# Kernel tuning notes

Measured on AMD Instinct MI355X. Metric: run time of the kernel, lower is better.

## Reference

```python
import jax, jax.numpy as jnp
import numpy as np

B, H, W = 64, 512, 512
T = 100           # num_thresholds
R = 8             # defect regions per image (max label id)
BLOCK = 128       # defect regions are 128x128 blocks on a 4x4 grid
SAT = 1.0         # saturation_threshold (relative)


def setup_inputs() -> dict:
    key = jax.random.key(0)
    k1, _ = jax.random.split(key)
    preds = jax.random.uniform(k1, (B, H, W), dtype=jnp.float32)
    thresholds = jnp.linspace(0.0, 1.0, T).astype(jnp.float32)
    # Build a labeled GT mask: R disjoint 128x128 block regions per image,
    # labels 1..R (0 = background). This plays the role of measure.label(target).
    rng = np.random.default_rng(0)
    labels = np.zeros((B, H, W), dtype=np.int32)
    gb = H // BLOCK           # 4 blocks per side -> 16 candidate blocks
    nblocks = gb * gb
    for b in range(B):
        chosen = rng.permutation(nblocks)[:R]
        for rid, blk in enumerate(chosen, start=1):
            r, c = divmod(int(blk), gb)
            labels[b, r * BLOCK:(r + 1) * BLOCK, c * BLOCK:(c + 1) * BLOCK] = rid
    return {"preds": preds, "thresholds": thresholds, "labels": jnp.asarray(labels)}


def reference(preds, thresholds, labels):
    # preds: (B,H,W) float32 in [0,1); thresholds: (T,) sorted; labels: (B,H,W) int32, 0=bg.
    Bn, Hn, Wn = preds.shape
    Tn = thresholds.shape[0]
    flat_s = preds.reshape(-1)
    flat_l = labels.reshape(-1)
    # bucket[p] = number of thresholds <= score[p]; pixel passes thr[t] iff bucket > t.
    bucket = jnp.searchsorted(thresholds, flat_s, side='right')  # int in [0, T]
    # ---- background FP / TN per threshold (exact counts via histogram) ----
    bg = (flat_l == 0).astype(jnp.int32)
    bg_hist = jax.ops.segment_sum(bg, bucket, num_segments=Tn + 1)  # (T+1,)
    bg_total = bg_hist.sum()
    fp = (bg_total - jnp.cumsum(bg_hist)[:Tn]).astype(jnp.float32)  # fp[t] = #bg with score>=thr[t]
    tn = bg_total.astype(jnp.float32) - fp
    # ---- per-region TP per threshold (segmented histogram) ----
    bidx = jnp.repeat(jnp.arange(Bn), Hn * Wn)
    seg = bidx * R + (flat_l - 1)              # region id in [0, B*R)
    comb = seg * (Tn + 1) + bucket
    NSEG = Bn * R * (Tn + 1)
    comb = jnp.where(flat_l > 0, comb, NSEG)   # dump bg pixels in overflow slot
    hist = jax.ops.segment_sum(jnp.ones_like(bucket, dtype=jnp.int32), comb,
                               num_segments=NSEG + 1)[:NSEG].reshape(Bn, R, Tn + 1)
    area = hist.sum(-1)                                       # (B,R) defect areas
    tp = (area[..., None] - jnp.cumsum(hist, -1)[..., :Tn]).astype(jnp.float32)  # (B,R,T)
    sat = jnp.maximum(area.astype(jnp.float32) * SAT, 1.0)    # relative saturation
    valid = (area > 0).astype(jnp.float32)                    # guard empty regions
    spro = jnp.minimum(tp / sat[..., None], 1.0) * valid[..., None]
    spro_sum = spro.sum((0, 1))                               # (T,)
    n_def = jnp.maximum(valid.sum(), 1.0)
    mean_spro = spro_sum / n_def
    # ---- AUC over FPR (max_fpr = 1.0) ----
    denom = fp + tn
    fpr = jnp.where(denom > 0, fp / jnp.maximum(denom, 1.0), 0.0)
    order = jnp.argsort(fpr)
    x = fpr[order]
    y = mean_spro[order]
    auc = jnp.sum((x[1:] - x[:-1]) * (y[1:] + y[:-1]) * 0.5)  # trapezoid rule
    return auc
```

## Files before the change

### kernel.cpp

```cpp
#include <hip/hip_runtime.h>

#define B_N 64
#define H_N 512
#define W_N 512
#define T_N 100
#define TB  101
#define R_N 8
#define NLAB 9
#define BLOCKS_PER_IMG 16
#define PIX_PER_IMG (H_N * W_N)
#define PIX_PER_BLOCK (PIX_PER_IMG / BLOCKS_PER_IMG)

__global__ __launch_bounds__(256) void hist_kernel(
    const float* __restrict__ preds, const int* __restrict__ labels,
    const float* __restrict__ thr,
    int* __restrict__ region_hist,
    int* __restrict__ bg_hist)
{
    __shared__ float s_thr[T_N];
    __shared__ int whist[4][NLAB * TB];

    const int tid  = threadIdx.x;
    const int wave = tid >> 6;

    for (int i = tid; i < 4 * NLAB * TB; i += 256) ((int*)whist)[i] = 0;
    if (tid < T_N) s_thr[tid] = thr[tid];
    __syncthreads();

    const int img   = blockIdx.x / BLOCKS_PER_IMG;
    const int chunk = blockIdx.x % BLOCKS_PER_IMG;
    const long base = (long)img * PIX_PER_IMG + (long)chunk * PIX_PER_BLOCK;
    const float4* p4 = (const float4*)(preds + base);
    const int4*   l4 = (const int4*)(labels + base);
    int* __restrict__ myh = whist[wave];

    const int iters = PIX_PER_BLOCK / (256 * 4);
    for (int it = 0; it < iters; ++it) {
        float4 pv = p4[it * 256 + tid];
        int4   lv = l4[it * 256 + tid];
        float ps[4] = {pv.x, pv.y, pv.z, pv.w};
        int   ls[4] = {lv.x, lv.y, lv.z, lv.w};
#pragma unroll
        for (int j = 0; j < 4; ++j) {
            float s = ps[j];
            int k = (int)(s * (float)(T_N - 1)) + 1;
            k = max(0, min(T_N, k));
            while (k < T_N && s_thr[k] <= s) ++k;
            while (k > 0 && s_thr[k - 1] > s) --k;
            atomicAdd(&myh[ls[j] * TB + k], 1);
        }
    }
    __syncthreads();

    for (int i = tid; i < NLAB * TB; i += 256) {
        int v = whist[0][i] + whist[1][i] + whist[2][i] + whist[3][i];
        if (v) {
            int lab = i / TB;
            int t   = i - lab * TB;
            if (lab == 0)
                atomicAdd(&bg_hist[img * TB + t], v);
            else
                atomicAdd(&region_hist[(img * R_N + (lab - 1)) * TB + t], v);
        }
    }
}

__global__ __launch_bounds__(128) void region_kernel(
    const int* __restrict__ region_hist,
    float* __restrict__ spro_sum,
    int* __restrict__ n_def)
{
    __shared__ float spro_sh[R_N][T_N];
    __shared__ int validc[R_N];
    const int img = blockIdx.x;
    const int tid = threadIdx.x;

    if (tid < R_N) {
        const int* h = &region_hist[(img * R_N + tid) * TB];
        int area = 0;
        for (int t = 0; t < TB; ++t) area += h[t];
        float sat   = fmaxf((float)area, 1.0f);
        float valid = (area > 0) ? 1.0f : 0.0f;
        int csum = 0;
        for (int t = 0; t < T_N; ++t) {
            csum += h[t];
            float tp = (float)(area - csum);
            spro_sh[tid][t] = fminf(tp / sat, 1.0f) * valid;
        }
        validc[tid] = (area > 0) ? 1 : 0;
    }
    __syncthreads();

    if (tid < T_N) {
        float s = 0.0f;
        for (int r = 0; r < R_N; ++r) s += spro_sh[r][tid];
        atomicAdd(&spro_sum[tid], s);
    }
    if (tid == 0) {
        int v = 0;
        for (int r = 0; r < R_N; ++r) v += validc[r];
        atomicAdd(n_def, v);
    }
}

__global__ __launch_bounds__(128) void final_kernel(
    const int* __restrict__ bg_hist,
    const float* __restrict__ spro_sum,
    const int* __restrict__ n_def,
    float* __restrict__ out)
{
    __shared__ int    bgh[TB];
    __shared__ float  fpr_sh[T_N];
    __shared__ float  ms_sh[T_N];
    __shared__ int    order[T_N];
    __shared__ double contrib[T_N];
    const int tid = threadIdx.x;

    if (tid < TB) {
        int s = 0;
        for (int b = 0; b < B_N; ++b) s += bg_hist[b * TB + tid];
        bgh[tid] = s;
    }
    __syncthreads();

    if (tid < T_N) {
        int fp_i = 0;
        for (int k = tid + 1; k < TB; ++k) fp_i += bgh[k];
        int tot = fp_i;
        for (int k = 0; k <= tid; ++k) tot += bgh[k];
        float bgt = (float)tot;
        float fp  = (float)fp_i;
        fpr_sh[tid] = (bgt > 0.0f) ? fp / fmaxf(bgt, 1.0f) : 0.0f;
        float nd = fmaxf((float)(*n_def), 1.0f);
        ms_sh[tid] = spro_sum[tid] / nd;
    }
    __syncthreads();

    if (tid < T_N) {
        float v = fpr_sh[tid];
        int r = 0;
        for (int j = 0; j < T_N; ++j) {
            float u = fpr_sh[j];
            r += (u < v) | ((u == v) & (j < tid));
        }
        order[r] = tid;
    }
    __syncthreads();

    if (tid < T_N - 1) {
        int o0 = order[tid], o1 = order[tid + 1];
        double x0 = fpr_sh[o0], x1 = fpr_sh[o1];
        double y0 = ms_sh[o0],  y1 = ms_sh[o1];
        contrib[tid] = (x1 - x0) * (y0 + y1) * 0.5;
    } else if (tid < T_N) {
        contrib[tid] = 0.0;
    }
    __syncthreads();

    if (tid == 0) {
        double s = 0.0;
        for (int i = 0; i < T_N - 1; ++i) s += contrib[i];
        out[0] = (float)s;
    }
}

extern "C" void kernel_launch(void* const* d_in, const int* in_sizes, int n_in,
                              void* d_out, int out_size, void* d_ws, size_t ws_size,
                              hipStream_t stream) {
    const float* preds  = (const float*)d_in[0];
    const float* thr    = (const float*)d_in[1];
    const int*   labels = (const int*)d_in[2];
    float* out = (float*)d_out;

    int*   region_hist = (int*)d_ws;
    int*   bg_hist     = region_hist + B_N * R_N * TB;
    float* spro_sum    = (float*)(bg_hist + B_N * TB);
    int*   n_def       = (int*)(spro_sum + T_N);

    size_t zbytes = sizeof(int) * (size_t)(B_N * R_N * TB + B_N * TB)
                  + sizeof(float) * T_N + sizeof(int);
    hipMemsetAsync(d_ws, 0, zbytes, stream);

    hist_kernel<<<B_N * BLOCKS_PER_IMG, 256, 0, stream>>>(preds, labels, thr,
                                                          region_hist, bg_hist);
    region_kernel<<<B_N, 128, 0, stream>>>(region_hist, spro_sum, n_def);
    final_kernel<<<1, 128, 0, stream>>>(bg_hist, spro_sum, n_def, out);
}
```

Baseline: 167.1 us.

## Use LUT bucket lookup, prefetch loads, more chunks, fuse tail kernels

The threshold search now goes through a 256-cell shared-memory table that gives the bucket with one comparison, falling back to a linear scan only near cell edges. The main loop double-buffers its global loads and splits each image into 32 chunks instead of 16, with a launch-bounds occupancy hint. The region and final kernels merge into one single-block tail kernel that reduces across waves with shuffles, removing a launch and the global atomics. The tail now runs on only one block, so its serial work may be slower.

```diff
diff --git a/kernel.cpp b/kernel.cpp
--- a/kernel.cpp
+++ b/kernel.cpp
@@ -7,48 +7,85 @@
 #define TB  101
 #define R_N 8
 #define NLAB 9
-#define BLOCKS_PER_IMG 16
+#define CHUNKS 32
 #define PIX_PER_IMG (H_N * W_N)
-#define PIX_PER_BLOCK (PIX_PER_IMG / BLOCKS_PER_IMG)
-
-__global__ __launch_bounds__(256) void hist_kernel(
+#define CPIX (PIX_PER_IMG / CHUNKS)
+#define NCELL 256
+
+struct LutE { float tlo, thrb, thi; int klo; };
+
+__global__ __launch_bounds__(256, 8) void hist_kernel(
     const float* __restrict__ preds, const int* __restrict__ labels,
     const float* __restrict__ thr,
     int* __restrict__ region_hist,
     int* __restrict__ bg_hist)
 {
     __shared__ float s_thr[T_N];
+    __shared__ __align__(16) LutE lut[NCELL];
     __shared__ int whist[4][NLAB * TB];
 
     const int tid  = threadIdx.x;
     const int wave = tid >> 6;
 
+    if (tid < T_N) s_thr[tid] = thr[tid];
     for (int i = tid; i < 4 * NLAB * TB; i += 256) ((int*)whist)[i] = 0;
-    if (tid < T_N) s_thr[tid] = thr[tid];
-    __syncthreads();
-
-    const int img   = blockIdx.x / BLOCKS_PER_IMG;
-    const int chunk = blockIdx.x % BLOCKS_PER_IMG;
-    const long base = (long)img * PIX_PER_IMG + (long)chunk * PIX_PER_BLOCK;
+    __syncthreads();
+
+    if (tid < NCELL) {
+        float lo = (float)tid * (1.0f / (float)NCELL);
+        int a = 0, b = T_N;
+        while (a < b) { int m = (a + b) >> 1; if (s_thr[m] <= lo) a = m + 1; else b = m; }
+        LutE e;
+        e.tlo  = (a > 0)       ? s_thr[a - 1] : -2.0f;
+        e.thrb = (a < T_N)     ? s_thr[a]     :  2.0f;
+        e.thi  = (a + 1 < T_N) ? s_thr[a + 1] :  2.0f;
+        e.klo  = a;
+        lut[tid] = e;
+    }
+    __syncthreads();
+
+    const int img   = blockIdx.x >> 5;
+    const int chunk = blockIdx.x & (CHUNKS - 1);
+    const long base = (long)img * PIX_PER_IMG + (long)chunk * CPIX;
     const float4* p4 = (const float4*)(preds + base);
     const int4*   l4 = (const int4*)(labels + base);
     int* __restrict__ myh = whist[wave];
 
-    const int iters = PIX_PER_BLOCK / (256 * 4);
-    for (int it = 0; it < iters; ++it) {
-        float4 pv = p4[it * 256 + tid];
-        int4   lv = l4[it * 256 + tid];
+    auto PROC = [&](float4 pv, int4 lv) {
         float ps[4] = {pv.x, pv.y, pv.z, pv.w};
         int   ls[4] = {lv.x, lv.y, lv.z, lv.w};
 #pragma unroll
         for (int j = 0; j < 4; ++j) {
             float s = ps[j];
-            int k = (int)(s * (float)(T_N - 1)) + 1;
-            k = max(0, min(T_N, k));
-            while (k < T_N && s_thr[k] <= s) ++k;
-            while (k > 0 && s_thr[k - 1] > s) --k;
+            int c = (int)(s * (float)NCELL);
+            c = max(0, min(NCELL - 1, c));
+            LutE e = lut[c];
+            bool ge = (s >= e.thrb);
+            int k = e.klo + (ge ? 1 : 0);
+            float lowv  = ge ? e.thrb : e.tlo;
+            float highv = ge ? e.thi  : e.thrb;
+            if (__builtin_expect(!(lowv <= s && s < highv), 0)) {
+                k = max(0, min(T_N, k));
+                while (k < T_N && s_thr[k] <= s) ++k;
+                while (k > 0 && s_thr[k - 1] > s) --k;
+            }
             atomicAdd(&myh[ls[j] * TB + k], 1);
         }
+    };
+
+    float4 pA0 = p4[0 * 256 + tid], pA1 = p4[1 * 256 + tid];
+    int4   lA0 = l4[0 * 256 + tid], lA1 = l4[1 * 256 + tid];
+#pragma unroll
+    for (int g = 0; g < 4; ++g) {
+        float4 pB0, pB1; int4 lB0, lB1;
+        if (g < 3) {
+            const int i0 = (g + 1) * 2;
+            pB0 = p4[(i0    ) * 256 + tid]; pB1 = p4[(i0 + 1) * 256 + tid];
+            lB0 = l4[(i0    ) * 256 + tid]; lB1 = l4[(i0 + 1) * 256 + tid];
+        }
+        __builtin_amdgcn_sched_barrier(0);
+        PROC(pA0, lA0); PROC(pA1, lA1);
+        pA0 = pB0; pA1 = pB1; lA0 = lB0; lA1 = lB1;
     }
     __syncthreads();
 
@@ -65,59 +102,51 @@
     }
 }
 
-__global__ __launch_bounds__(128) void region_kernel(
+__global__ __launch_bounds__(256) void tail_kernel(
     const int* __restrict__ region_hist,
-    float* __restrict__ spro_sum,
-    int* __restrict__ n_def)
-{
-    __shared__ float spro_sh[R_N][T_N];
-    __shared__ int validc[R_N];
-    const int img = blockIdx.x;
-    const int tid = threadIdx.x;
-
-    if (tid < R_N) {
-        const int* h = &region_hist[(img * R_N + tid) * TB];
-        int area = 0;
-        for (int t = 0; t < TB; ++t) area += h[t];
-        float sat   = fmaxf((float)area, 1.0f);
-        float valid = (area > 0) ? 1.0f : 0.0f;
-        int csum = 0;
-        for (int t = 0; t < T_N; ++t) {
-            csum += h[t];
-            float tp = (float)(area - csum);
-            spro_sh[tid][t] = fminf(tp / sat, 1.0f) * valid;
-        }
-        validc[tid] = (area > 0) ? 1 : 0;
-    }
-    __syncthreads();
-
-    if (tid < T_N) {
-        float s = 0.0f;
-        for (int r = 0; r < R_N; ++r) s += spro_sh[r][tid];
-        atomicAdd(&spro_sum[tid], s);
-    }
-    if (tid == 0) {
-        int v = 0;
-        for (int r = 0; r < R_N; ++r) v += validc[r];
-        atomicAdd(n_def, v);
-    }
-}
-
-__global__ __launch_bounds__(128) void final_kernel(
     const int* __restrict__ bg_hist,
-    const float* __restrict__ spro_sum,
-    const int* __restrict__ n_def,
     float* __restrict__ out)
 {
+    __shared__ float  spro_acc[T_N];
+    __shared__ int    nd_acc;
     __shared__ int    bgh[TB];
     __shared__ float  fpr_sh[T_N];
     __shared__ float  ms_sh[T_N];
     __shared__ int    order[T_N];
     __shared__ double contrib[T_N];
-    const int tid = threadIdx.x;
+
+    const int tid  = threadIdx.x;
+    const int lane = tid & 63;
+
+    if (tid < T_N) spro_acc[tid] = 0.0f;
+    if (tid == 0) nd_acc = 0;
+    __syncthreads();
+
+    const int* h0 = region_hist + tid * TB;
+    const int* h1 = region_hist + (tid + 256) * TB;
+    int area0 = 0, area1 = 0;
+#pragma unroll 4
+    for (int t = 0; t < TB; ++t) { area0 += h0[t]; area1 += h1[t]; }
+    const float sat0 = fmaxf((float)area0, 1.0f);
+    const float sat1 = fmaxf((float)area1, 1.0f);
+    const float val0 = (area0 > 0) ? 1.0f : 0.0f;
+    const float val1 = (area1 > 0) ? 1.0f : 0.0f;
+    atomicAdd(&nd_acc, (area0 > 0 ? 1 : 0) + (area1 > 0 ? 1 : 0));
+
+    int cs0 = 0, cs1 = 0;
+#pragma unroll 4
+    for (int t = 0; t < T_N; ++t) {
+        cs0 += h0[t]; cs1 += h1[t];
+        float c = fminf((float)(area0 - cs0) / sat0, 1.0f) * val0
+                + fminf((float)(area1 - cs1) / sat1, 1.0f) * val1;
+#pragma unroll
+        for (int off = 32; off; off >>= 1) c += __shfl_down(c, off, 64);
+        if (lane == 0) atomicAdd(&spro_acc[t], c);
+    }
 
     if (tid < TB) {
         int s = 0;
+#pragma unroll 4
         for (int b = 0; b < B_N; ++b) s += bg_hist[b * TB + tid];
         bgh[tid] = s;
     }
@@ -129,10 +158,8 @@
         int tot = fp_i;
         for (int k = 0; k <= tid; ++k) tot += bgh[k];
         float bgt = (float)tot;
-        float fp  = (float)fp_i;
-        fpr_sh[tid] = (bgt > 0.0f) ? fp / fmaxf(bgt, 1.0f) : 0.0f;
-        float nd = fmaxf((float)(*n_def), 1.0f);
-        ms_sh[tid] = spro_sum[tid] / nd;
+        fpr_sh[tid] = (bgt > 0.0f) ? (float)fp_i / fmaxf(bgt, 1.0f) : 0.0f;
+        ms_sh[tid]  = spro_acc[tid] / fmaxf((float)nd_acc, 1.0f);
     }
     __syncthreads();
 
@@ -140,8 +167,8 @@
         float v = fpr_sh[tid];
         int r = 0;
         for (int j = 0; j < T_N; ++j) {
-            float u = fpr_sh[j];
-            r += (u < v) | ((u == v) & (j < tid));
+            float w = fpr_sh[j];
+            r += (w < v) | ((w == v) & (j < tid));
         }
         order[r] = tid;
     }
@@ -172,17 +199,13 @@
     const int*   labels = (const int*)d_in[2];
     float* out = (float*)d_out;
 
-    int*   region_hist = (int*)d_ws;
-    int*   bg_hist     = region_hist + B_N * R_N * TB;
-    float* spro_sum    = (float*)(bg_hist + B_N * TB);
-    int*   n_def       = (int*)(spro_sum + T_N);
-
-    size_t zbytes = sizeof(int) * (size_t)(B_N * R_N * TB + B_N * TB)
-                  + sizeof(float) * T_N + sizeof(int);
+    int* region_hist = (int*)d_ws;
+    int* bg_hist     = region_hist + B_N * R_N * TB;
+
+    size_t zbytes = sizeof(int) * (size_t)(B_N * R_N * TB + B_N * TB);
     hipMemsetAsync(d_ws, 0, zbytes, stream);
 
-    hist_kernel<<<B_N * BLOCKS_PER_IMG, 256, 0, stream>>>(preds, labels, thr,
-                                                          region_hist, bg_hist);
-    region_kernel<<<B_N, 128, 0, stream>>>(region_hist, spro_sum, n_def);
-    final_kernel<<<1, 128, 0, stream>>>(bg_hist, spro_sum, n_def, out);
+    hist_kernel<<<B_N * CHUNKS, 256, 0, stream>>>(preds, labels, thr,
+                                                  region_hist, bg_hist);
+    tail_kernel<<<1, 256, 0, stream>>>(region_hist, bg_hist, out);
 }
```

New measurement: 215.7 us. +29.0%, slower.
